# Kernel tuning notes

Hardware: AMD Instinct MI355X
Metric: run time of the kernel (lower is better)

## Reference

```python
import jax, jax.numpy as jnp
import numpy as np

B, N, H = 32, 2048, 256          # batch, num_docs, hidden_dim
F_HEADS = 8                      # config.dynamic_fusion_heads
NH = 8                           # num_heads inside each nn.MultiheadAttention
STEPS = 3                        # config.meta_adaptation_steps


def setup_inputs() -> dict:
    key = jax.random.key(0)
    ks = jax.random.split(key, 10)
    s = 0.02
    return {
        "query": jax.random.normal(ks[0], (B, H), jnp.float32),
        "retrieved_docs": jax.random.normal(ks[1], (B, N, H), jnp.float32),
        "causal_weights": jax.random.uniform(ks[2], (B, N, 1), jnp.float32),
        "context_history": jax.random.normal(ks[3], (B, H), jnp.float32),
        # per-fusion-head MultiheadAttention params (torch layout: in_proj [3H,H])
        "in_proj_w": jax.random.normal(ks[4], (F_HEADS, 3 * H, H), jnp.float32) * s,
        "in_proj_b": jnp.zeros((F_HEADS, 3 * H), jnp.float32),
        "out_proj_w": jax.random.normal(ks[5], (F_HEADS, H, H), jnp.float32) * s,
        "out_proj_b": jnp.zeros((F_HEADS, H), jnp.float32),
        "strategy_w": jax.random.normal(ks[6], (F_HEADS, H), jnp.float32) * s,
        "strategy_b": jnp.zeros((F_HEADS,), jnp.float32),
        "meta_params": jax.random.normal(ks[7], (STEPS, H, H), jnp.float32) * 0.02,
    }


def _mha_qlen1(q, kv, Wi, bi, Wo, bo):
    # q: [B,H] (query length 1), kv: [B,N,H]. Torch MHA semantics, batch_first.
    Wq, Wk, Wv = jnp.split(Wi, 3, axis=0)
    bq, bk, bv = jnp.split(bi, 3)
    dh = H // NH
    qh = (q @ Wq.T + bq).reshape(B, NH, dh)
    kh = (kv @ Wk.T + bk).reshape(B, N, NH, dh)
    vh = (kv @ Wv.T + bv).reshape(B, N, NH, dh)
    scores = jnp.einsum('bhd,bnhd->bhn', qh, kh) / jnp.sqrt(jnp.float32(dh))
    attn = jax.nn.softmax(scores, axis=-1)
    ctx = jnp.einsum('bhn,bnhd->bhd', attn, vh).reshape(B, H)
    return ctx @ Wo.T + bo


def reference(query, retrieved_docs, causal_weights, context_history,
              in_proj_w, in_proj_b, out_proj_w, out_proj_b,
              strategy_w, strategy_b, meta_params):
    # causal weighting of retrieved docs (shared across all fusion heads)
    weighted_docs = retrieved_docs * causal_weights  # [B,N,H]

    # batch all 8 fusion heads' cross-attention in one vmapped pass -> [F,B,H]
    heads_out = jax.vmap(
        lambda Wi, bi, Wo, bo: _mha_qlen1(query, weighted_docs, Wi, bi, Wo, bo)
    )(in_proj_w, in_proj_b, out_proj_w, out_proj_b)

    # sequential residual meta-adaptation steps (same matrices for every head)
    for i in range(STEPS):
        heads_out = heads_out + heads_out @ meta_params[i]

    # strategy-weighted combine of fusion heads
    strategy = jax.nn.softmax(query @ strategy_w.T + strategy_b, axis=-1)  # [B,F]
    return jnp.einsum('fbh,bf->bh', heads_out, strategy)  # [B,H]
```

## Files before the change

### kernel.cpp

```cpp
#include <hip/hip_runtime.h>
#include <hip/hip_bf16.h>


#define B_ 32
#define N_ 2048
#define H_ 256
#define F_ 8
#define FH_ 64
#define NCH_ 8

typedef unsigned short u16;
typedef __attribute__((ext_vector_type(8))) short bf16x8;
typedef __attribute__((ext_vector_type(4))) float f32x4;
#define MFMA(a, b, c) __builtin_amdgcn_mfma_f32_16x16x32_bf16((a), (b), (c), 0, 0, 0)

__device__ __forceinline__ u16 f2b(float x) {
  unsigned u = __builtin_bit_cast(unsigned, x);
  return (u16)((u + 0x7fffu + ((u >> 16) & 1u)) >> 16);
}
__device__ __forceinline__ float b2f(u16 h) {
  unsigned u = ((unsigned)h) << 16;
  return __builtin_bit_cast(float, u);
}

static constexpr size_t UB_U     = 0;
static constexpr size_t UB_W     = 1048576;
static constexpr size_t UB_L     = 3145728;
static constexpr size_t UB_STRAT = 3153920;
static constexpr size_t UB_MT    = 3154944;

__global__ __launch_bounds__(512) void k1_fused(
    const float* __restrict__ query, const float* __restrict__ ipw,
    const float* __restrict__ ipb, const float* __restrict__ stw,
    const float* __restrict__ stb, const float* __restrict__ meta,
    u16* __restrict__ u, u16* __restrict__ metaT, float* __restrict__ strat)
{
  const int tid = threadIdx.x, L = tid & 63, w = tid >> 6;
  const int khi = L >> 4, col = L & 15;

  if (blockIdx.x >= 16) {
    const int bid2 = blockIdx.x - 16;
    const int s = bid2 >> 3, x0 = (bid2 & 7) * 32;
    __shared__ u16 sT[32 * 264];
    #pragma unroll
    for (int p = 0; p < 4; ++p) {
      int idx = tid + 512 * p;
      int r = idx >> 3, xq = (idx & 7) * 4;
      float4 v = *(const float4*)&meta[((size_t)(s * 256) + r) * 256 + x0 + xq];
      sT[(xq + 0) * 264 + r] = f2b(v.x);
      sT[(xq + 1) * 264 + r] = f2b(v.y);
      sT[(xq + 2) * 264 + r] = f2b(v.z);
      sT[(xq + 3) * 264 + r] = f2b(v.w);
    }
    __syncthreads();
    #pragma unroll
    for (int p = 0; p < 2; ++p) {
      int idx = tid + 512 * p;
      int x = idx >> 5, rq = (idx & 31) * 8;
      bf16x8 v = *(bf16x8*)&sT[x * 264 + rq];
      *(bf16x8*)&metaT[((size_t)(s * 256) + x0 + x) * 256 + rq] = v;
    }
    return;
  }

  const int f = blockIdx.x >> 1, hf = blockIdx.x & 1;
  __shared__ u16 sW[256 * 40];
  __shared__ u16 qhh[32 * 136];
  __shared__ u16 qhl[32 * 136];
  __shared__ float slog[256];

  bf16x8 qf[2][8];
  #pragma unroll
  for (int bt = 0; bt < 2; ++bt)
    #pragma unroll
    for (int ks = 0; ks < 8; ++ks) {
      const float* qp = &query[(size_t)(bt * 16 + col) * H_ + ks * 32 + khi * 8];
      float4 v0 = *(const float4*)qp, v1 = *(const float4*)(qp + 4);
      bf16x8 q;
      q[0] = f2b(v0.x); q[1] = f2b(v0.y); q[2] = f2b(v0.z); q[3] = f2b(v0.w);
      q[4] = f2b(v1.x); q[5] = f2b(v1.y); q[6] = f2b(v1.z); q[7] = f2b(v1.w);
      qf[bt][ks] = q;
    }

  if (f == 0 && hf == 0 && w == 0) {
    f32x4 sacc[2] = {(f32x4){0.f,0.f,0.f,0.f}, (f32x4){0.f,0.f,0.f,0.f}};
    #pragma unroll
    for (int ks = 0; ks < 8; ++ks) {
      bf16x8 a = (bf16x8){0,0,0,0,0,0,0,0};
      if (col < 8) {
        const float* sp = &stw[(size_t)col * H_ + ks * 32 + khi * 8];
        float4 v0 = *(const float4*)sp, v1 = *(const float4*)(sp + 4);
        a[0] = f2b(v0.x); a[1] = f2b(v0.y); a[2] = f2b(v0.z); a[3] = f2b(v0.w);
        a[4] = f2b(v1.x); a[5] = f2b(v1.y); a[6] = f2b(v1.z); a[7] = f2b(v1.w);
      }
      sacc[0] = MFMA(a, qf[0][ks], sacc[0]);
      sacc[1] = MFMA(a, qf[1][ks], sacc[1]);
    }
    if (khi < 2) {
      #pragma unroll
      for (int bt = 0; bt < 2; ++bt)
        #pragma unroll
        for (int r = 0; r < 4; ++r) {
          int i = khi * 4 + r;
          slog[(bt * 16 + col) * 8 + i] = sacc[bt][r] + stb[i];
        }
    }
  }

  f32x4 qacc[2] = {(f32x4){0.f,0.f,0.f,0.f}, (f32x4){0.f,0.f,0.f,0.f}};
  for (int ks = 0; ks < 8; ++ks) {
    #pragma unroll
    for (int p = 0; p < 2; ++p) {
      int gid = tid + 512 * p;
      int r = gid >> 3, kq = (gid & 7) * 4;
      float4 v = *(const float4*)&ipw[((size_t)(f * 768) + hf * 128 + r) * H_ + ks * 32 + kq];
      *(ushort4*)&sW[r * 40 + kq] = make_ushort4(f2b(v.x), f2b(v.y), f2b(v.z), f2b(v.w));
    }
    __syncthreads();
    bf16x8 a = *(const bf16x8*)&sW[(w * 16 + col) * 40 + khi * 8];
    qacc[0] = MFMA(a, qf[0][ks], qacc[0]);
    qacc[1] = MFMA(a, qf[1][ks], qacc[1]);
    __syncthreads();
  }
  {
    int r0 = w * 16 + khi * 4;
    float4 bq = *(const float4*)&ipb[f * 768 + hf * 128 + r0];
    #pragma unroll
    for (int bt = 0; bt < 2; ++bt) {
      int b = bt * 16 + col;
      float v0 = qacc[bt][0] + bq.x, v1 = qacc[bt][1] + bq.y;
      float v2 = qacc[bt][2] + bq.z, v3 = qacc[bt][3] + bq.w;
      ushort4 hs = make_ushort4(f2b(v0), f2b(v1), f2b(v2), f2b(v3));
      ushort4 ls = make_ushort4(f2b(v0 - b2f(hs.x)), f2b(v1 - b2f(hs.y)),
                                f2b(v2 - b2f(hs.z)), f2b(v3 - b2f(hs.w)));
      *(ushort4*)&qhh[b * 136 + r0] = hs;
      *(ushort4*)&qhl[b * 136 + r0] = ls;
    }
  }
  __syncthreads();

  if (f == 0 && hf == 0 && tid < 32) {
    float mx = slog[tid * 8];
    #pragma unroll
    for (int i = 1; i < F_; ++i) mx = fmaxf(mx, slog[tid * 8 + i]);
    float s = 0.f, e[F_];
    #pragma unroll
    for (int i = 0; i < F_; ++i) { e[i] = __expf(slog[tid * 8 + i] - mx); s += e[i]; }
    #pragma unroll
    for (int i = 0; i < F_; ++i) strat[tid * F_ + i] = e[i] / s;
  }

  const float scale = 0.17677669529663687f;
  for (int hh = 0; hh < 4; ++hh) {
    #pragma unroll
    for (int p = 0; p < 4; ++p) {
      int gid = tid + 512 * p;
      int d = gid >> 6, jq = (gid & 63) * 4;
      float4 v = *(const float4*)&ipw[((size_t)(f * 768 + 256) + (hf * 4 + hh) * 32 + d) * H_ + jq];
      float vv[4] = {v.x, v.y, v.z, v.w};
      #pragma unroll
      for (int e = 0; e < 4; ++e) {
        int j = jq + e;
        sW[j * 40 + (d ^ (((j >> 4) & 3) << 3))] = f2b(vv[e]);
      }
    }
    __syncthreads();
    #pragma unroll
    for (int q = 0; q < 2; ++q) {
      int jt = w * 2 + q;
      bf16x8 a = *(const bf16x8*)&sW[(jt * 16 + col) * 40 + ((khi ^ (jt & 3)) * 8)];
      #pragma unroll
      for (int bt = 0; bt < 2; ++bt) {
        int b = bt * 16 + col;
        bf16x8 bh = *(const bf16x8*)&qhh[b * 136 + hh * 32 + khi * 8];
        bf16x8 bl = *(const bf16x8*)&qhl[b * 136 + hh * 32 + khi * 8];
        f32x4 acc = (f32x4){0.f, 0.f, 0.f, 0.f};
        acc = MFMA(a, bh, acc);
        acc = MFMA(a, bl, acc);
        int j0 = jt * 16 + khi * 4;
        ushort4 us = make_ushort4(f2b(acc[0] * scale), f2b(acc[1] * scale),
                                  f2b(acc[2] * scale), f2b(acc[3] * scale));
        *(ushort4*)&u[((size_t)(b * 64) + f * 8 + hf * 4 + hh) * H_ + j0] = us;
      }
    }
    __syncthreads();
  }
}

__global__ __launch_bounds__(512) void k4_one(
    const float* __restrict__ docs, const float* __restrict__ cw,
    const u16* __restrict__ u, float* __restrict__ wbuf, float* __restrict__ lbuf)
{
  const int ns = blockIdx.x, b = blockIdx.y;
  const int n0 = ns * 256;
  const int tid = threadIdx.x, L = tid & 63, w = tid >> 6;
  const int khi = L >> 4, col = L & 15;
  const int ft = w & 3, nt0 = (w >> 2) * 2;

  __shared__ u16 sdu[64 * 264];
  __shared__ u16 phu[64 * 72];
  __shared__ u16 plou[64 * 72];

  bf16x8 uf[8];
  #pragma unroll
  for (int ks = 0; ks < 8; ++ks)
    uf[ks] = *(const bf16x8*)&u[((size_t)(b * 64) + ft * 16 + col) * H_ + ks * 32 + khi * 8];

  float4 dv[8];
  #pragma unroll
  for (int p = 0; p < 8; ++p) {
    int idx = tid + 512 * p;
    int n = idx >> 6, jq = (idx & 63) * 4;
    dv[p] = *(const float4*)&docs[((size_t)(b * N_) + n0 + n) * H_ + jq];
  }
  #pragma unroll
  for (int p = 0; p < 8; ++p) {
    int idx = tid + 512 * p;
    int n = idx >> 6, jq = (idx & 63) * 4;
    *(ushort4*)&sdu[n * 264 + (jq ^ (((n >> 3) & 3) << 4))] =
        make_ushort4(f2b(dv[p].x), f2b(dv[p].y), f2b(dv[p].z), f2b(dv[p].w));
  }
  __syncthreads();

  f32x4 acc2[4][2];
  #pragma unroll
  for (int mt = 0; mt < 4; ++mt)
    #pragma unroll
    for (int jt = 0; jt < 2; ++jt) acc2[mt][jt] = (f32x4){0.f, 0.f, 0.f, 0.f};
  float eacc[4] = {0.f, 0.f, 0.f, 0.f};

  for (int nc = 0; nc < 4; ++nc) {
    if (nc < 3) {
      #pragma unroll
      for (int p = 0; p < 8; ++p) {
        int idx = tid + 512 * p;
        int n = idx >> 6, jq = (idx & 63) * 4;
        dv[p] = *(const float4*)&docs[((size_t)(b * N_) + n0 + (nc + 1) * 64 + n) * H_ + jq];
      }
    }
    f32x4 sc0 = (f32x4){0.f, 0.f, 0.f, 0.f}, sc1 = sc0;
    const int nr0 = nt0 * 16 + col, nr1 = (nt0 + 1) * 16 + col;
    const int sw0 = ((nr0 >> 3) & 3) << 4, sw1 = ((nr1 >> 3) & 3) << 4;
    #pragma unroll
    for (int ks = 0; ks < 8; ++ks) {
      bf16x8 b0 = *(const bf16x8*)&sdu[nr0 * 264 + ((ks * 32 + khi * 8) ^ sw0)];
      bf16x8 b1 = *(const bf16x8*)&sdu[nr1 * 264 + ((ks * 32 + khi * 8) ^ sw1)];
      sc0 = MFMA(uf[ks], b0, sc0);
      sc1 = MFMA(uf[ks], b1, sc1);
    }
    {
      int ng = n0 + nc * 64 + nt0 * 16 + col;
      float cv0 = cw[(size_t)b * N_ + ng];
      float cv1 = cw[(size_t)b * N_ + ng + 16];
      #pragma unroll
      for (int r = 0; r < 4; ++r) {
        int fh = ft * 16 + khi * 4 + r;
        float ex0 = __expf(sc0[r] * cv0);
        float ex1 = __expf(sc1[r] * cv1);
        eacc[r] += ex0 + ex1;
        float p0 = ex0 * cv0, p1 = ex1 * cv1;
        u16 h0 = f2b(p0), h1 = f2b(p1);
        phu [fh * 72 + nt0 * 16 + col]       = h0;
        plou[fh * 72 + nt0 * 16 + col]       = f2b(p0 - b2f(h0));
        phu [fh * 72 + (nt0 + 1) * 16 + col] = h1;
        plou[fh * 72 + (nt0 + 1) * 16 + col] = f2b(p1 - b2f(h1));
      }
    }
    __syncthreads();

    #pragma unroll
    for (int kk = 0; kk < 2; ++kk) {
      #pragma unroll
      for (int jt = 0; jt < 2; ++jt) {
        int j = w * 32 + jt * 16 + col;
        bf16x8 bb;
        #pragma unroll
        for (int jj = 0; jj < 8; ++jj)
          bb[jj] = (short)sdu[(kk * 32 + khi * 8 + jj) * 264 + (j ^ (khi << 4))];
        #pragma unroll
        for (int mt = 0; mt < 4; ++mt) {
          bf16x8 ah = *(const bf16x8*)&phu [(mt * 16 + col) * 72 + kk * 32 + khi * 8];
          bf16x8 al = *(const bf16x8*)&plou[(mt * 16 + col) * 72 + kk * 32 + khi * 8];
          acc2[mt][jt] = MFMA(ah, bb, acc2[mt][jt]);
          acc2[mt][jt] = MFMA(al, bb, acc2[mt][jt]);
        }
      }
    }
    __syncthreads();

    if (nc < 3) {
      #pragma unroll
      for (int p = 0; p < 8; ++p) {
        int idx = tid + 512 * p;
        int n = idx >> 6, jq = (idx & 63) * 4;
        *(ushort4*)&sdu[n * 264 + (jq ^ (((n >> 3) & 3) << 4))] =
            make_ushort4(f2b(dv[p].x), f2b(dv[p].y), f2b(dv[p].z), f2b(dv[p].w));
      }
      __syncthreads();
    }
  }
  #pragma unroll
  for (int mt = 0; mt < 4; ++mt)
    #pragma unroll
    for (int jt = 0; jt < 2; ++jt)
      #pragma unroll
      for (int r = 0; r < 4; ++r) {
        int fh = mt * 16 + khi * 4 + r;
        int j = w * 32 + jt * 16 + col;
        atomicAdd(&wbuf[((size_t)(b * 64) + fh) * H_ + j], acc2[mt][jt][r]);
      }
  #pragma unroll
  for (int r = 0; r < 4; ++r) {
    float e = eacc[r];
    e += __shfl_xor(e, 1, 64);
    e += __shfl_xor(e, 2, 64);
    e += __shfl_xor(e, 4, 64);
    e += __shfl_xor(e, 8, 64);
    if (col == 0)
      atomicAdd(&lbuf[(size_t)(b * 64) + ft * 16 + khi * 4 + r], e);
  }
}

__global__ __launch_bounds__(512) void k5_mfma(
    const float* __restrict__ ipw, const float* __restrict__ ipb,
    const float* __restrict__ opw, const float* __restrict__ opb,
    const u16* __restrict__ metaT, const float* __restrict__ wbuf,
    const float* __restrict__ lbuf, const float* __restrict__ strat,
    float* __restrict__ out)
{
  const int f = blockIdx.x & 7, b0 = (blockIdx.x >> 3) * 16;
  const int tid = threadIdx.x, L = tid & 63, w = tid >> 6;
  const int khi = L >> 4, col = L & 15;

  __shared__ char smem[57856];
  __shared__ float sli[128];
  u16* sWvP  = (u16*)(smem);
  u16* sWhiP = (u16*)(smem + 20480);
  u16* sWloP = (u16*)(smem + 30720);
  u16* sWo   = (u16*)(smem);
  u16* XBh   = (u16*)(smem + 20480);
  u16* XBl   = (u16*)(smem + 28928);
  u16* XAh   = (u16*)(smem + 40960);
  u16* XAl   = (u16*)(smem + 49408);

  if (tid < 128)
    sli[tid] = 1.f / lbuf[(size_t)((b0 + (tid & 15)) * 64) + f * 8 + (tid >> 4)];
  __syncthreads();

  f32x4 cacc0 = (f32x4){0.f, 0.f, 0.f, 0.f};
  f32x4 cacc1 = (f32x4){0.f, 0.f, 0.f, 0.f};
  for (int ks = 0; ks < 8; ++ks) {
    #pragma unroll
    for (int p = 0; p < 4; ++p) {
      int idx = tid + 512 * p;
      int r = idx >> 3, cq = (idx & 7) * 4;
      float4 v = *(const float4*)&ipw[((size_t)(f * 768 + 512) + r) * 256 + ks * 32 + cq];
      *(ushort4*)&sWvP[r * 40 + cq] = make_ushort4(f2b(v.x), f2b(v.y), f2b(v.z), f2b(v.w));
    }
    #pragma unroll
    for (int p = 0; p < 2; ++p) {
      int idx = tid + 512 * p;
      int rr = idx >> 3, cq = (idx & 7) * 4;
      int h = rr >> 4, b = rr & 15;
      float li = sli[rr];
      float4 v = *(const float4*)&wbuf[((size_t)((b0 + b) * 64) + f * 8 + h) * 256 + ks * 32 + cq];
      v.x *= li; v.y *= li; v.z *= li; v.w *= li;
      u16 hx = f2b(v.x), hy = f2b(v.y), hz = f2b(v.z), hw2 = f2b(v.w);
      *(ushort4*)&sWhiP[rr * 40 + cq] = make_ushort4(hx, hy, hz, hw2);
      *(ushort4*)&sWloP[rr * 40 + cq] = make_ushort4(
          f2b(v.x - b2f(hx)), f2b(v.y - b2f(hy)), f2b(v.z - b2f(hz)), f2b(v.w - b2f(hw2)));
    }
    __syncthreads();
    bf16x8 bh = *(bf16x8*)&sWhiP[(w * 16 + col) * 40 + khi * 8];
    bf16x8 bl = *(bf16x8*)&sWloP[(w * 16 + col) * 40 + khi * 8];
    bf16x8 a0 = *(bf16x8*)&sWvP[(w * 32 + col) * 40 + khi * 8];
    bf16x8 a1 = *(bf16x8*)&sWvP[(w * 32 + 16 + col) * 40 + khi * 8];
    cacc0 = MFMA(a0, bh, cacc0); cacc0 = MFMA(a0, bl, cacc0);
    cacc1 = MFMA(a1, bh, cacc1); cacc1 = MFMA(a1, bl, cacc1);
    __syncthreads();
  }
  #pragma unroll
  for (int mt = 0; mt < 2; ++mt) {
    f32x4 cv = mt ? cacc1 : cacc0;
    #pragma unroll
    for (int r = 0; r < 4; ++r) {
      int d = mt * 16 + khi * 4 + r;
      float vv = cv[r] + ipb[f * 768 + 512 + w * 32 + d];
      u16 hi = f2b(vv);
      XAh[col * 264 + w * 32 + d] = hi;
      XAl[col * 264 + w * 32 + d] = f2b(vv - b2f(hi));
    }
  }

  f32x4 hr0, hr1;
  {
    float bo0 = opb[f * 256 + (w * 2 + 0) * 16 + col];
    float bo1 = opb[f * 256 + (w * 2 + 1) * 16 + col];
    hr0 = (f32x4){bo0, bo0, bo0, bo0};
    hr1 = (f32x4){bo1, bo1, bo1, bo1};
  }
  for (int ks = 0; ks < 8; ++ks) {
    #pragma unroll
    for (int p = 0; p < 4; ++p) {
      int idx = tid + 512 * p;
      int r = idx >> 3, cq = (idx & 7) * 4;
      float4 v = *(const float4*)&opw[((size_t)(f * 256) + r) * 256 + ks * 32 + cq];
      *(ushort4*)&sWo[r * 40 + cq] = make_ushort4(f2b(v.x), f2b(v.y), f2b(v.z), f2b(v.w));
    }
    __syncthreads();
    bf16x8 ah  = *(bf16x8*)&XAh[col * 264 + ks * 32 + khi * 8];
    bf16x8 al  = *(bf16x8*)&XAl[col * 264 + ks * 32 + khi * 8];
    bf16x8 bw0 = *(bf16x8*)&sWo[((w * 2 + 0) * 16 + col) * 40 + khi * 8];
    bf16x8 bw1 = *(bf16x8*)&sWo[((w * 2 + 1) * 16 + col) * 40 + khi * 8];
    hr0 = MFMA(ah, bw0, hr0); hr0 = MFMA(al, bw0, hr0);
    hr1 = MFMA(ah, bw1, hr1); hr1 = MFMA(al, bw1, hr1);
    __syncthreads();
  }

  auto spill = [&](u16* Oh, u16* Ol) {
    #pragma unroll
    for (int q = 0; q < 2; ++q) {
      f32x4 hv = q ? hr1 : hr0;
      int x = (w * 2 + q) * 16 + col;
      #pragma unroll
      for (int r = 0; r < 4; ++r) {
        u16 hi = f2b(hv[r]);
        Oh[(khi * 4 + r) * 264 + x] = hi;
        Ol[(khi * 4 + r) * 264 + x] = f2b(hv[r] - b2f(hi));
      }
    }
  };
  auto meta_mm = [&](const u16* Ah_, const u16* Al_, int s) {
    f32x4 n0 = hr0, n1 = hr1;
    #pragma unroll
    for (int ks = 0; ks < 8; ++ks) {
      bf16x8 ah = *(const bf16x8*)&Ah_[col * 264 + ks * 32 + khi * 8];
      bf16x8 al = *(const bf16x8*)&Al_[col * 264 + ks * 32 + khi * 8];
      const u16* mrow = &metaT[((size_t)(s * 256) + (w * 2) * 16 + col) * 256 + ks * 32 + khi * 8];
      bf16x8 m0 = *(const bf16x8*)mrow;
      bf16x8 m1 = *(const bf16x8*)(mrow + 16 * 256);
      n0 = MFMA(ah, m0, n0); n0 = MFMA(al, m0, n0);
      n1 = MFMA(ah, m1, n1); n1 = MFMA(al, m1, n1);
    }
    hr0 = n0; hr1 = n1;
  };

  spill(XBh, XBl);
  __syncthreads();
  meta_mm(XBh, XBl, 0);
  spill(XAh, XAl);
  __syncthreads();
  meta_mm(XAh, XAl, 1);
  spill(XBh, XBl);
  __syncthreads();
  meta_mm(XBh, XBl, 2);

  #pragma unroll
  for (int q = 0; q < 2; ++q) {
    f32x4 hv = q ? hr1 : hr0;
    int x = (w * 2 + q) * 16 + col;
    #pragma unroll
    for (int r = 0; r < 4; ++r) {
      int b = khi * 4 + r;
      float sv = strat[(b0 + b) * F_ + f];
      atomicAdd(&out[(size_t)(b0 + b) * H_ + x], sv * hv[r]);
    }
  }
}

extern "C" void kernel_launch(void* const* d_in, const int* in_sizes, int n_in,
                              void* d_out, int out_size, void* d_ws, size_t ws_size,
                              hipStream_t stream) {
  const float* query = (const float*)d_in[0];
  const float* docs  = (const float*)d_in[1];
  const float* cw    = (const float*)d_in[2];
  const float* ipw   = (const float*)d_in[4];
  const float* ipb   = (const float*)d_in[5];
  const float* opw   = (const float*)d_in[6];
  const float* opb   = (const float*)d_in[7];
  const float* stw   = (const float*)d_in[8];
  const float* stb   = (const float*)d_in[9];
  const float* meta  = (const float*)d_in[10];
  float* out = (float*)d_out;

  char* base = (char*)d_ws;
  u16*   u     = (u16*)(base + UB_U);
  float* wbuf  = (float*)(base + UB_W);
  float* lbuf  = (float*)(base + UB_L);
  float* strat = (float*)(base + UB_STRAT);
  u16*   metaT = (u16*)(base + UB_MT);

  hipMemsetAsync(out, 0, (size_t)B_ * H_ * sizeof(float), stream);
  hipMemsetAsync(base + UB_W, 0,
                 (size_t)(B_ * FH_ * H_ * sizeof(float) + B_ * FH_ * sizeof(float)),
                 stream);
  k1_fused<<<dim3(40), 512, 0, stream>>>(query, ipw, ipb, stw, stb, meta, u, metaT, strat);
  k4_one<<<dim3(NCH_, B_), 512, 0, stream>>>(docs, cw, u, wbuf, lbuf);
  k5_mfma<<<dim3(16), 512, 0, stream>>>(ipw, ipb, opw, opb, metaT, wbuf, lbuf, strat, out);
}
```

Before: 195.6 us.

## Load k5 weight fragments directly into registers instead of staging through LDS

In k5, the V-projection weights, the normalized wbuf context rows and the out-projection weights are now loaded from global memory straight into MFMA operand registers and converted to bf16 in registers. This replaces the old per-k-step shared-memory staging, which needed two barriers per step. The goal is to remove the LDS round trips and barrier stalls in these two GEMM phases. In exchange, register pressure rises because 32 bf16x8 fragments are held per thread, and the global loads are less coalesced since each lane reads its own row segment.

```diff
diff --git a/kernel.cpp b/kernel.cpp
--- a/kernel.cpp
+++ b/kernel.cpp
@@ -21,6 +21,13 @@
 __device__ __forceinline__ float b2f(u16 h) {
   unsigned u = ((unsigned)h) << 16;
   return __builtin_bit_cast(float, u);
+}
+__device__ __forceinline__ bf16x8 ld8b(const float* p) {
+  float4 v0 = *(const float4*)p, v1 = *(const float4*)(p + 4);
+  bf16x8 a;
+  a[0] = f2b(v0.x); a[1] = f2b(v0.y); a[2] = f2b(v0.z); a[3] = f2b(v0.w);
+  a[4] = f2b(v1.x); a[5] = f2b(v1.y); a[6] = f2b(v1.z); a[7] = f2b(v1.w);
+  return a;
 }
 
 static constexpr size_t UB_U     = 0;
@@ -73,26 +80,15 @@
   #pragma unroll
   for (int bt = 0; bt < 2; ++bt)
     #pragma unroll
-    for (int ks = 0; ks < 8; ++ks) {
-      const float* qp = &query[(size_t)(bt * 16 + col) * H_ + ks * 32 + khi * 8];
-      float4 v0 = *(const float4*)qp, v1 = *(const float4*)(qp + 4);
-      bf16x8 q;
-      q[0] = f2b(v0.x); q[1] = f2b(v0.y); q[2] = f2b(v0.z); q[3] = f2b(v0.w);
-      q[4] = f2b(v1.x); q[5] = f2b(v1.y); q[6] = f2b(v1.z); q[7] = f2b(v1.w);
-      qf[bt][ks] = q;
-    }
+    for (int ks = 0; ks < 8; ++ks)
+      qf[bt][ks] = ld8b(&query[(size_t)(bt * 16 + col) * H_ + ks * 32 + khi * 8]);
 
   if (f == 0 && hf == 0 && w == 0) {
     f32x4 sacc[2] = {(f32x4){0.f,0.f,0.f,0.f}, (f32x4){0.f,0.f,0.f,0.f}};
     #pragma unroll
     for (int ks = 0; ks < 8; ++ks) {
       bf16x8 a = (bf16x8){0,0,0,0,0,0,0,0};
-      if (col < 8) {
-        const float* sp = &stw[(size_t)col * H_ + ks * 32 + khi * 8];
-        float4 v0 = *(const float4*)sp, v1 = *(const float4*)(sp + 4);
-        a[0] = f2b(v0.x); a[1] = f2b(v0.y); a[2] = f2b(v0.z); a[3] = f2b(v0.w);
-        a[4] = f2b(v1.x); a[5] = f2b(v1.y); a[6] = f2b(v1.z); a[7] = f2b(v1.w);
-      }
+      if (col < 8) a = ld8b(&stw[(size_t)col * H_ + ks * 32 + khi * 8]);
       sacc[0] = MFMA(a, qf[0][ks], sacc[0]);
       sacc[1] = MFMA(a, qf[1][ks], sacc[1]);
     }
@@ -332,52 +328,35 @@
   const int tid = threadIdx.x, L = tid & 63, w = tid >> 6;
   const int khi = L >> 4, col = L & 15;
 
-  __shared__ char smem[57856];
-  __shared__ float sli[128];
-  u16* sWvP  = (u16*)(smem);
-  u16* sWhiP = (u16*)(smem + 20480);
-  u16* sWloP = (u16*)(smem + 30720);
-  u16* sWo   = (u16*)(smem);
-  u16* XBh   = (u16*)(smem + 20480);
-  u16* XBl   = (u16*)(smem + 28928);
-  u16* XAh   = (u16*)(smem + 40960);
-  u16* XAl   = (u16*)(smem + 49408);
-
-  if (tid < 128)
-    sli[tid] = 1.f / lbuf[(size_t)((b0 + (tid & 15)) * 64) + f * 8 + (tid >> 4)];
-  __syncthreads();
-
+  __shared__ u16 XAh[16 * 264], XAl[16 * 264];
+  __shared__ u16 XBh[16 * 264], XBl[16 * 264];
+
+  bf16x8 av[2][8];
+  #pragma unroll
+  for (int mt = 0; mt < 2; ++mt)
+    #pragma unroll
+    for (int ks = 0; ks < 8; ++ks)
+      av[mt][ks] = ld8b(&ipw[((size_t)(f * 768 + 512) + w * 32 + mt * 16 + col) * H_
+                             + ks * 32 + khi * 8]);
+  const size_t wrow = ((size_t)((b0 + col) * 64) + f * 8 + w) * H_;
+  const float li = 1.f / lbuf[(size_t)((b0 + col) * 64) + f * 8 + w];
   f32x4 cacc0 = (f32x4){0.f, 0.f, 0.f, 0.f};
   f32x4 cacc1 = (f32x4){0.f, 0.f, 0.f, 0.f};
+  #pragma unroll
   for (int ks = 0; ks < 8; ++ks) {
-    #pragma unroll
-    for (int p = 0; p < 4; ++p) {
-      int idx = tid + 512 * p;
-      int r = idx >> 3, cq = (idx & 7) * 4;
-      float4 v = *(const float4*)&ipw[((size_t)(f * 768 + 512) + r) * 256 + ks * 32 + cq];
-      *(ushort4*)&sWvP[r * 40 + cq] = make_ushort4(f2b(v.x), f2b(v.y), f2b(v.z), f2b(v.w));
-    }
-    #pragma unroll
-    for (int p = 0; p < 2; ++p) {
-      int idx = tid + 512 * p;
-      int rr = idx >> 3, cq = (idx & 7) * 4;
-      int h = rr >> 4, b = rr & 15;
-      float li = sli[rr];
-      float4 v = *(const float4*)&wbuf[((size_t)((b0 + b) * 64) + f * 8 + h) * 256 + ks * 32 + cq];
-      v.x *= li; v.y *= li; v.z *= li; v.w *= li;
-      u16 hx = f2b(v.x), hy = f2b(v.y), hz = f2b(v.z), hw2 = f2b(v.w);
-      *(ushort4*)&sWhiP[rr * 40 + cq] = make_ushort4(hx, hy, hz, hw2);
-      *(ushort4*)&sWloP[rr * 40 + cq] = make_ushort4(
-          f2b(v.x - b2f(hx)), f2b(v.y - b2f(hy)), f2b(v.z - b2f(hz)), f2b(v.w - b2f(hw2)));
-    }
-    __syncthreads();
-    bf16x8 bh = *(bf16x8*)&sWhiP[(w * 16 + col) * 40 + khi * 8];
-    bf16x8 bl = *(bf16x8*)&sWloP[(w * 16 + col) * 40 + khi * 8];
-    bf16x8 a0 = *(bf16x8*)&sWvP[(w * 32 + col) * 40 + khi * 8];
-    bf16x8 a1 = *(bf16x8*)&sWvP[(w * 32 + 16 + col) * 40 + khi * 8];
-    cacc0 = MFMA(a0, bh, cacc0); cacc0 = MFMA(a0, bl, cacc0);
-    cacc1 = MFMA(a1, bh, cacc1); cacc1 = MFMA(a1, bl, cacc1);
-    __syncthreads();
+    const float* p = &wbuf[wrow + ks * 32 + khi * 8];
+    float4 v0 = *(const float4*)p, v1 = *(const float4*)(p + 4);
+    float vv[8] = {v0.x, v0.y, v0.z, v0.w, v1.x, v1.y, v1.z, v1.w};
+    bf16x8 bh, bl;
+    #pragma unroll
+    for (int e = 0; e < 8; ++e) {
+      float x = vv[e] * li;
+      u16 h = f2b(x);
+      bh[e] = (short)h;
+      bl[e] = (short)f2b(x - b2f(h));
+    }
+    cacc0 = MFMA(av[0][ks], bh, cacc0); cacc0 = MFMA(av[0][ks], bl, cacc0);
+    cacc1 = MFMA(av[1][ks], bh, cacc1); cacc1 = MFMA(av[1][ks], bl, cacc1);
   }
   #pragma unroll
   for (int mt = 0; mt < 2; ++mt) {
@@ -392,6 +371,15 @@
     }
   }
 
+  bf16x8 bw[2][8];
+  #pragma unroll
+  for (int q = 0; q < 2; ++q)
+    #pragma unroll
+    for (int ks = 0; ks < 8; ++ks)
+      bw[q][ks] = ld8b(&opw[((size_t)(f * 256) + (w * 2 + q) * 16 + col) * H_
+                            + ks * 32 + khi * 8]);
+  __syncthreads();
+
   f32x4 hr0, hr1;
   {
     float bo0 = opb[f * 256 + (w * 2 + 0) * 16 + col];
@@ -399,22 +387,12 @@
     hr0 = (f32x4){bo0, bo0, bo0, bo0};
     hr1 = (f32x4){bo1, bo1, bo1, bo1};
   }
+  #pragma unroll
   for (int ks = 0; ks < 8; ++ks) {
-    #pragma unroll
-    for (int p = 0; p < 4; ++p) {
-      int idx = tid + 512 * p;
-      int r = idx >> 3, cq = (idx & 7) * 4;
-      float4 v = *(const float4*)&opw[((size_t)(f * 256) + r) * 256 + ks * 32 + cq];
-      *(ushort4*)&sWo[r * 40 + cq] = make_ushort4(f2b(v.x), f2b(v.y), f2b(v.z), f2b(v.w));
-    }
-    __syncthreads();
-    bf16x8 ah  = *(bf16x8*)&XAh[col * 264 + ks * 32 + khi * 8];
-    bf16x8 al  = *(bf16x8*)&XAl[col * 264 + ks * 32 + khi * 8];
-    bf16x8 bw0 = *(bf16x8*)&sWo[((w * 2 + 0) * 16 + col) * 40 + khi * 8];
-    bf16x8 bw1 = *(bf16x8*)&sWo[((w * 2 + 1) * 16 + col) * 40 + khi * 8];
-    hr0 = MFMA(ah, bw0, hr0); hr0 = MFMA(al, bw0, hr0);
-    hr1 = MFMA(ah, bw1, hr1); hr1 = MFMA(al, bw1, hr1);
-    __syncthreads();
+    bf16x8 ah = *(const bf16x8*)&XAh[col * 264 + ks * 32 + khi * 8];
+    bf16x8 al = *(const bf16x8*)&XAl[col * 264 + ks * 32 + khi * 8];
+    hr0 = MFMA(ah, bw[0][ks], hr0); hr0 = MFMA(al, bw[0][ks], hr0);
+    hr1 = MFMA(ah, bw[1][ks], hr1); hr1 = MFMA(al, bw[1][ks], hr1);
   }
 
   auto spill = [&](u16* Oh, u16* Ol) {
```

Result: no change. 192.6 us (-1.6%).
